# Kernel optimization log

Measured on AMD Instinct MI355X. Metric: run time of the kernel, lower is better.

Reference implementation:

```python
import jax, jax.numpy as jnp
import numpy as np

H = 16      # num_heads = num_channels // head_dim
D = 128     # head_dim
BLK = 64    # NABLA / flex_attention block size
THR = 0.8   # sparse_params['P'] cumulative-density threshold
EPS = 1e-6  # RMSNorm eps


def _rmsnorm(x, w):
    # torch nn.RMSNorm over last dim (computed in fp32 as in norm_qk)
    return x * jax.lax.rsqrt(jnp.mean(x * x, axis=-1, keepdims=True) + EPS) * w


def _rotate_half(x):
    x1, x2 = jnp.split(x, 2, axis=-1)
    return jnp.concatenate([-x2, x1], axis=-1)


def _apply_rotary(x, cos, sin):
    # x: [S, H, D]; cos/sin: [S, 1, D]
    return x * cos + _rotate_half(x) * sin


def _nabla_block_mask(q, k, sta_mask):
    # q, k: [H, S, D] -> block-pooled attention map, cumulative-density threshold
    Hh, S, Dd = q.shape
    nb = S // BLK
    qb = q.reshape(Hh, nb, BLK, Dd).mean(axis=2)           # [H, nQ, D]
    kb = k.reshape(Hh, nb, BLK, Dd).mean(axis=2)           # [H, nK, D]
    p = jax.nn.softmax(jnp.einsum('hqd,hkd->hqk', qb, kb) / np.sqrt(Dd), axis=-1)
    srt = -jnp.sort(-p, axis=-1)                           # descending
    csum = jnp.cumsum(srt, axis=-1)
    keep_sorted = (csum - srt) < THR                       # smallest set covering THR mass
    cutoff = jnp.min(jnp.where(keep_sorted, srt, jnp.inf), axis=-1, keepdims=True)
    return (p >= cutoff) | sta_mask[None]                  # [H, nQ, nK] bool


def reference(x, rope_cos, rope_sin, sta_mask, Wq, bq, Wk, bk, Wv, bv, Wo, bo, qn_w, kn_w):
    S, C = x.shape
    q = (x @ Wq + bq).reshape(S, H, D)
    k = (x @ Wk + bk).reshape(S, H, D)
    v = (x @ Wv + bv).reshape(S, H, D)
    q = _rmsnorm(q, qn_w)
    k = _rmsnorm(k, kn_w)
    q = _apply_rotary(q, rope_cos, rope_sin)
    k = _apply_rotary(k, rope_cos, rope_sin)
    q = q.transpose(1, 0, 2)  # [H, S, D]
    k = k.transpose(1, 0, 2)
    v = v.transpose(1, 0, 2)
    blk_keep = _nabla_block_mask(q, k, sta_mask)                     # [H, nQ, nK]
    mask = jnp.repeat(jnp.repeat(blk_keep, BLK, axis=1), BLK, axis=2)  # [H, S, S]
    scores = jnp.einsum('hqd,hkd->hqk', q, k) / np.sqrt(D)
    scores = jnp.where(mask, scores, -jnp.inf)
    attn = jax.nn.softmax(scores, axis=-1)
    out = jnp.einsum('hqk,hkd->hqd', attn, v)                        # [H, S, D]
    out = out.transpose(1, 0, 2).reshape(S, H * D)
    return out @ Wo + bo


def setup_inputs() -> dict:
    key = jax.random.key(0)
    ks = jax.random.split(key, 12)
    S, C = 2048, 2048
    nb = S // BLK
    sc = 0.02
    return {
        'x': jax.random.normal(ks[0], (S, C), jnp.float32),
        'rope_cos': jax.random.uniform(ks[1], (S, 1, D), jnp.float32),
        'rope_sin': jax.random.uniform(ks[2], (S, 1, D), jnp.float32),
        'sta_mask': jax.random.randint(ks[3], (nb, nb), 0, 2).astype(bool),
        'Wq': jax.random.normal(ks[4], (C, C), jnp.float32) * sc,
        'bq': jnp.zeros((C,), jnp.float32),
        'Wk': jax.random.normal(ks[5], (C, C), jnp.float32) * sc,
        'bk': jnp.zeros((C,), jnp.float32),
        'Wv': jax.random.normal(ks[6], (C, C), jnp.float32) * sc,
        'bv': jnp.zeros((C,), jnp.float32),
        'Wo': jax.random.normal(ks[7], (C, C), jnp.float32) * sc,
        'bo': jnp.zeros((C,), jnp.float32),
        'qn_w': jnp.ones((D,), jnp.float32),
        'kn_w': jnp.ones((D,), jnp.float32),
    }
```

## Files before the change

### kernel.cpp

```cpp
#include <hip/hip_runtime.h>


#define S_LEN 2048
#define CDIM  2048
#define NH    16
#define HD    128
#define NB    32

typedef __attribute__((ext_vector_type(8))) short s8v;
typedef __attribute__((ext_vector_type(4))) short s4v;
typedef __attribute__((ext_vector_type(4))) float f4v;

__device__ __forceinline__ short f2bf(float f){
  unsigned u = __builtin_bit_cast(unsigned, f);
  u += 0x7fffu + ((u>>16)&1u);
  return (short)(u>>16);
}
__device__ __forceinline__ float bf2f(short s){
  unsigned u = ((unsigned)(unsigned short)s)<<16;
  return __builtin_bit_cast(float, u);
}
__device__ __forceinline__ void gload_lds16(const void* g, void* l){
  __builtin_amdgcn_global_load_lds(
      (const __attribute__((address_space(1))) void*)g,
      (__attribute__((address_space(3))) void*)l, 16, 0, 0);
}

__global__ void __launch_bounds__(256) conv_x_kernel(
    const float* __restrict__ x, short* __restrict__ xcat)
{
  int i = blockIdx.x*256 + threadIdx.x;
  f4v v = ((const f4v*)x)[i];
  int s = i >> 9, c4 = (i & 511)*4;
  s4v hi, lo;
#pragma unroll
  for (int e=0;e<4;e++){
    short h = f2bf(v[e]);
    hi[e] = h;
    lo[e] = f2bf(v[e] - bf2f(h));
  }
  short* row = xcat + (size_t)s*6144 + c4;
  *(s4v*)(row)        = hi;
  *(s4v*)(row + 2048) = hi;
  *(s4v*)(row + 4096) = lo;
}

__global__ void __launch_bounds__(256) conv_w3_kernel(
    const float* __restrict__ W, short* __restrict__ wcat)
{
  __shared__ float tile[64][65];
  const int k0 = blockIdx.y*64, n0 = blockIdx.x*64, t = threadIdx.x;
#pragma unroll
  for (int i=0;i<16;i++){
    int idx = i*256 + t, r = idx>>6, c = idx&63;
    tile[r][c] = W[(size_t)(k0+r)*2048 + (n0+c)];
  }
  __syncthreads();
#pragma unroll
  for (int i=0;i<16;i++){
    int idx = i*256 + t, n = idx>>6, k = idx&63;
    float v = tile[k][n];
    short h  = f2bf(v);
    short lo = f2bf(v - bf2f(h));
    short* base = wcat + (size_t)(n0+n)*6144 + (k0+k);
    base[0]    = h;
    base[2048] = lo;
    base[4096] = h;
  }
}

__global__ void __launch_bounds__(256) conv_w1_kernel(
    const float* __restrict__ W, short* __restrict__ wt)
{
  __shared__ float tile[64][65];
  const int k0 = blockIdx.y*64, n0 = blockIdx.x*64, t = threadIdx.x;
#pragma unroll
  for (int i=0;i<16;i++){
    int idx = i*256 + t, r = idx>>6, c = idx&63;
    tile[r][c] = W[(size_t)(k0+r)*2048 + (n0+c)];
  }
  __syncthreads();
#pragma unroll
  for (int i=0;i<16;i++){
    int idx = i*256 + t, n = idx>>6, k = idx&63;
    wt[(size_t)(n0+n)*2048 + (k0+k)] = f2bf(tile[k][n]);
  }
}

template<int OUT>
__global__ void __launch_bounds__(512, 4) gemm8_bt(
    const short* __restrict__ A, int lda,
    const short* __restrict__ Bt, int ldb,
    const float* __restrict__ biasQ, const float* __restrict__ biasK,
    int nsplit,
    void* __restrict__ Cout, int ldc, int K, int ntiles)
{
  __shared__ short Alds[2][128*64];
  __shared__ short Blds[2][128*64];
  const int t = threadIdx.x, w = t>>6, l = t&63;
  const int nwg = gridDim.x;
  const int bid = blockIdx.x;
  const int swz = (bid & 7)*(nwg>>3) + (bid>>3);
  const int mi = swz / ntiles, ni = swz % ntiles;
  const int m0 = mi*128, n0 = ni*128;
  const int wr = w>>2, wc = w&3;
  const int l16 = l&15, lg = l>>4;

  f4v acc[4][2];
  f4v z = {0.f,0.f,0.f,0.f};
#pragma unroll
  for (int a=0;a<4;a++)
#pragma unroll
    for (int b=0;b<2;b++) acc[a][b] = z;

  const int srow = w*16 + (l>>3);
  const int scol = ((l&7) ^ ((l>>3)&7)) * 8;
  const short* Ag = A  + (size_t)(m0 + srow)*lda + scol;
  const short* Bg = Bt + (size_t)(n0 + srow)*ldb + scol;

  auto stageAB = [&](int buf, int kt){
#pragma unroll
    for (int ii=0;ii<2;ii++){
      gload_lds16(Ag + (size_t)ii*8*lda + kt, (char*)Alds[buf] + w*2048 + ii*1024);
      gload_lds16(Bg + (size_t)ii*8*ldb + kt, (char*)Blds[buf] + w*2048 + ii*1024);
    }
  };

  stageAB(0, 0);
  int cur = 0;
  for (int kt = 0; kt < K; kt += 64){
    if (kt + 64 < K){
      stageAB(cur^1, kt+64);
      asm volatile("s_waitcnt vmcnt(4)" ::: "memory");
    } else {
      asm volatile("s_waitcnt vmcnt(0)" ::: "memory");
    }
    __builtin_amdgcn_s_barrier();
    const char* Al = (const char*)Alds[cur];
    const char* Bl = (const char*)Blds[cur];
#pragma unroll
    for (int kk=0;kk<2;kk++){
      const int swx = ((l16&7)<<4);
      s8v af[4], bfv[2];
#pragma unroll
      for (int mt=0;mt<4;mt++)
        af[mt]  = *(const s8v*)(Al + (wr*64+mt*16+l16)*128 + ((kk*64 + lg*16) ^ swx));
#pragma unroll
      for (int jt=0;jt<2;jt++)
        bfv[jt] = *(const s8v*)(Bl + (wc*32+jt*16+l16)*128 + ((kk*64 + lg*16) ^ swx));
      __builtin_amdgcn_s_setprio(1);
#pragma unroll
      for (int mt=0;mt<4;mt++)
#pragma unroll
        for (int jt=0;jt<2;jt++)
          acc[mt][jt] = __builtin_amdgcn_mfma_f32_16x16x32_bf16(
              af[mt], bfv[jt], acc[mt][jt], 0, 0, 0);
      __builtin_amdgcn_s_setprio(0);
    }
    asm volatile("" ::: "memory");
    __builtin_amdgcn_s_barrier();
    cur ^= 1;
  }

  const float* bp = (n0 >= nsplit) ? (biasK + (n0 - nsplit)) : (biasQ + n0);

#pragma unroll
  for (int mt=0;mt<4;mt++)
#pragma unroll
    for (int r=0;r<4;r++){
      int row = m0 + wr*64 + mt*16 + lg*4 + r;
#pragma unroll
      for (int jt=0;jt<2;jt++){
        int cr = wc*32 + jt*16 + l16;
        float v = acc[mt][jt][r] + bp[cr];
        if (OUT == 0) ((float*)Cout)[(size_t)row*ldc + n0 + cr] = v;
        else          ((short*)Cout)[(size_t)row*ldc + n0 + cr] = f2bf(v);
      }
    }
}

__global__ void __launch_bounds__(256) qk_post_kernel(
    const float* __restrict__ QKf,
    const float* __restrict__ qw, const float* __restrict__ kw,
    const float* __restrict__ rc, const float* __restrict__ rs,
    short* __restrict__ Qh, short* __restrict__ Kh,
    float* __restrict__ Qb, float* __restrict__ Kb)
{
  __shared__ float pool[4][128];
  const int sb = blockIdx.x, h = blockIdx.y, which = blockIdx.z;
  const float* in    = QKf + (which ? 2048 : 0);
  const float* wvp   = which ? kw : qw;
  short*       outp  = which ? Kh : Qh;
  float*       poolp = which ? Kb : Qb;
  const int t = threadIdx.x, w = t>>6, l = t&63;
  const int s = sb*64 + w*16 + (l>>2), d0 = (l&3)*32;

  float a[32];
  const f4v* src = (const f4v*)(in + (size_t)s*4096 + h*128 + d0);
#pragma unroll
  for (int i=0;i<8;i++){
    f4v v = src[i];
    a[i*4]=v[0]; a[i*4+1]=v[1]; a[i*4+2]=v[2]; a[i*4+3]=v[3];
  }
  float ss = 0.f;
#pragma unroll
  for (int i=0;i<32;i++) ss += a[i]*a[i];
  ss += __shfl_xor(ss,1); ss += __shfl_xor(ss,2);
  float rstd = 1.0f / sqrtf(ss*(1.0f/128.0f) + 1e-6f);

  const f4v* wv4 = (const f4v*)(wvp + d0);
#pragma unroll
  for (int i=0;i<8;i++){
    f4v wv = wv4[i];
    a[i*4]   *= rstd*wv[0]; a[i*4+1] *= rstd*wv[1];
    a[i*4+2] *= rstd*wv[2]; a[i*4+3] *= rstd*wv[3];
  }
  float cv[32], sv[32];
  const f4v* cs4 = (const f4v*)(rc + (size_t)s*128 + d0);
  const f4v* sn4 = (const f4v*)(rs + (size_t)s*128 + d0);
#pragma unroll
  for (int i=0;i<8;i++){
    f4v c = cs4[i], sn = sn4[i];
    cv[i*4]=c[0]; cv[i*4+1]=c[1]; cv[i*4+2]=c[2]; cv[i*4+3]=c[3];
    sv[i*4]=sn[0]; sv[i*4+1]=sn[1]; sv[i*4+2]=sn[2]; sv[i*4+3]=sn[3];
  }
  const float sgn = (l&2) ? 1.f : -1.f;
#pragma unroll
  for (int i=0;i<32;i++){
    float pv = __shfl_xor(a[i], 2);
    a[i] = a[i]*cv[i] + sgn*pv*sv[i];
  }
  short* op = outp + ((size_t)h*2048 + s)*128 + d0;
#pragma unroll
  for (int c8=0;c8<8;c8++){
    s4v ob;
#pragma unroll
    for (int e=0;e<4;e++) ob[e] = f2bf(a[c8*4+e]);
    ((s4v*)op)[c8] = ob;
  }
#pragma unroll
  for (int i=0;i<32;i++){
    a[i] += __shfl_xor(a[i],4);
    a[i] += __shfl_xor(a[i],8);
    a[i] += __shfl_xor(a[i],16);
    a[i] += __shfl_xor(a[i],32);
  }
  if ((l>>2)==0){
#pragma unroll
    for (int i=0;i<32;i++) pool[w][d0+i] = a[i];
  }
  __syncthreads();
  if (t < 128)
    poolp[((size_t)h*32 + sb)*128 + t] =
        (pool[0][t]+pool[1][t]+pool[2][t]+pool[3][t]) * (1.0f/64.0f);
}

__global__ void __launch_bounds__(64) nabla_mask_kernel(
    const float* __restrict__ Qb, const float* __restrict__ Kb,
    const void* __restrict__ sta, unsigned char* __restrict__ keep)
{
  const int qi = blockIdx.x, h = blockIdx.y, l = threadIdx.x;
  const int j = l & 31;
  const int* si = (const int*)sta;
  int wv0 = si[j];
  int isInt = __all((wv0==0) | (wv0==1));

  const f4v* qr = (const f4v*)(Qb + ((size_t)h*32+qi)*128);
  const f4v* kr = (const f4v*)(Kb + ((size_t)h*32+j)*128);
  float dot = 0.f;
#pragma unroll
  for (int d=0; d<32; d++){
    f4v a = qr[d], b = kr[d];
    dot += a[0]*b[0] + a[1]*b[1] + a[2]*b[2] + a[3]*b[3];
  }
  float logit = dot / sqrtf(128.0f);
  float mx = logit;
  mx = fmaxf(mx, __shfl_xor(mx,1));  mx = fmaxf(mx, __shfl_xor(mx,2));
  mx = fmaxf(mx, __shfl_xor(mx,4));  mx = fmaxf(mx, __shfl_xor(mx,8));
  mx = fmaxf(mx, __shfl_xor(mx,16));
  float e = expf(logit - mx);
  float den = e;
  den += __shfl_xor(den,1);  den += __shfl_xor(den,2);
  den += __shfl_xor(den,4);  den += __shfl_xor(den,8);
  den += __shfl_xor(den,16);
  float p = e / den;
  float Sg = 0.f;
  for (int jj=0;jj<32;jj++){
    float pj = __shfl(p, jj);
    if (pj > p) Sg += pj;
  }
  float cand = (Sg < 0.8f) ? p : 3.0e38f;
  float cut = cand;
  cut = fminf(cut, __shfl_xor(cut,1));  cut = fminf(cut, __shfl_xor(cut,2));
  cut = fminf(cut, __shfl_xor(cut,4));  cut = fminf(cut, __shfl_xor(cut,8));
  cut = fminf(cut, __shfl_xor(cut,16));
  bool stab = isInt ? (si[qi*32+j] != 0)
                    : (((const unsigned char*)sta)[qi*32+j] != 0);
  if (l < 32)
    keep[((size_t)(h*32)+qi)*32 + j] = ((p >= cut) || stab) ? 1 : 0;
}

__global__ void __launch_bounds__(256) v_trans_kernel(
    const short* __restrict__ v_sd, short* __restrict__ vt)
{
  __shared__ short tile[64][65];
  const int sb = blockIdx.x, db = blockIdx.y, h = blockIdx.z, t = threadIdx.x;
#pragma unroll
  for (int i=0;i<16;i++){
    int idx = i*256 + t, r = idx>>6, c = idx&63;
    tile[r][c] = v_sd[(size_t)(sb*64+r)*2048 + h*128 + db*64 + c];
  }
  __syncthreads();
#pragma unroll
  for (int i=0;i<16;i++){
    int idx = i*256 + t, dn = idx>>6, s2 = idx&63;
    vt[((size_t)h*128 + db*64 + dn)*2048 + sb*64 + s2] = tile[s2][dn];
  }
}

__global__ void __launch_bounds__(256) attn_fwd_kernel(
    const short* __restrict__ qh, const short* __restrict__ kh,
    const short* __restrict__ vt, const unsigned char* __restrict__ keep,
    short* __restrict__ attn_out)
{
  __shared__ short Klds[2][64*128];
  __shared__ short Vlds[2][128*64];
  __shared__ short Plds[4][1024];
  const int bid = blockIdx.x;
  const int swz = (bid & 7)*64 + (bid >> 3);
  const int h = swz >> 5, qb = swz & 31;
  const int t = threadIdx.x, w = t>>6, l = t&63;
  const int l16 = l&15, lg = l>>4;

  s8v qf[4];
  const int sq0 = qb*64 + w*16;
  const short* qbase = qh + ((size_t)h*2048 + sq0 + l16)*128 + lg*8;
#pragma unroll
  for (int kf=0;kf<4;kf++) qf[kf] = *(const s8v*)(qbase + kf*32);

  f4v acc[8];
  f4v z = {0.f,0.f,0.f,0.f};
#pragma unroll
  for (int d=0;d<8;d++) acc[d] = z;
  float mrow[4], lsum[4];
#pragma unroll
  for (int r=0;r<4;r++){ mrow[r] = -3.0e38f; lsum[r] = 0.f; }

  const unsigned char* keeprow = keep + ((size_t)(h*32) + qb)*32;
  const short* kg0 = kh + (size_t)h*2048*128;
  const short* vg0 = vt + (size_t)h*128*2048;

  unsigned km = 0;
#pragma unroll
  for (int j=0;j<32;j++) km |= ((unsigned)keeprow[j]) << j;
  if (!km) km = 1;

  auto stageKV = [&](int buf, int j){
    const char* kg = (const char*)(kg0 + (size_t)(j*64)*128);
    const char* vg = (const char*)(vg0 + j*64);
#pragma unroll
    for (int ii=0;ii<4;ii++){
      int kr = (w*4+ii)*4 + (l>>4);
      int ks = ((l&15)*16) ^ ((kr&7)<<4);
      gload_lds16(kg + (size_t)kr*256 + ks, (char*)Klds[buf] + (w*4+ii)*1024);
      int vr = (w*4+ii)*8 + (l>>3);
      int vs = ((l&7)*16) ^ ((vr&7)<<4);
      gload_lds16(vg + (size_t)vr*4096 + vs, (char*)Vlds[buf] + (w*4+ii)*1024);
    }
  };

  asm volatile("s_waitcnt vmcnt(0)" ::: "memory");
  int jcur = (int)__builtin_ctz(km); km &= km-1;
  stageKV(0, jcur);
  int cur = 0;

  while (jcur >= 0){
    int jn = -1;
    if (km){ jn = (int)__builtin_ctz(km); km &= km-1; }
    if (jn >= 0){
      stageKV(cur^1, jn);
      asm volatile("s_waitcnt vmcnt(8)" ::: "memory");
    } else {
      asm volatile("s_waitcnt vmcnt(0)" ::: "memory");
    }
    __builtin_amdgcn_s_barrier();

    const char* Kl = (const char*)Klds[cur];
    const char* Vl = (const char*)Vlds[cur];

    f4v sacc[4];
#pragma unroll
    for (int nt=0;nt<4;nt++) sacc[nt] = z;
    __builtin_amdgcn_s_setprio(1);
#pragma unroll
    for (int kf=0;kf<4;kf++)
#pragma unroll
      for (int nt=0;nt<4;nt++){
        int kr = nt*16 + l16;
        s8v bfr = *(const s8v*)(Kl + ((kr*256 + kf*64 + lg*16) ^ ((kr&7)<<4)));
        sacc[nt] = __builtin_amdgcn_mfma_f32_16x16x32_bf16(qf[kf], bfr, sacc[nt], 0,0,0);
      }
    __builtin_amdgcn_s_setprio(0);
    const float scl = 0.08838834764831845f;
#pragma unroll
    for (int nt=0;nt<4;nt++) sacc[nt] *= scl;

#pragma unroll
    for (int r=0;r<4;r++){
      float mx = fmaxf(fmaxf(sacc[0][r], sacc[1][r]),
                       fmaxf(sacc[2][r], sacc[3][r]));
      mx = fmaxf(mx, __shfl_xor(mx,1));  mx = fmaxf(mx, __shfl_xor(mx,2));
      mx = fmaxf(mx, __shfl_xor(mx,4));  mx = fmaxf(mx, __shfl_xor(mx,8));
      float mnew = fmaxf(mrow[r], mx);
      float resc = __expf(mrow[r] - mnew);
      mrow[r] = mnew;
      float psum = 0.f;
#pragma unroll
      for (int nt=0;nt<4;nt++){
        float p = __expf(sacc[nt][r] - mnew);
        sacc[nt][r] = p;
        psum += p;
      }
      psum += __shfl_xor(psum,1);  psum += __shfl_xor(psum,2);
      psum += __shfl_xor(psum,4);  psum += __shfl_xor(psum,8);
      lsum[r] = lsum[r]*resc + psum;
#pragma unroll
      for (int dt=0;dt<8;dt++) acc[dt][r] *= resc;
    }

    char* Pl = (char*)Plds[w];
#pragma unroll
    for (int nt=0;nt<4;nt++)
#pragma unroll
      for (int r=0;r<4;r++){
        int pr = lg*4 + r;
        *(short*)(Pl + ((pr*128 + nt*32 + l16*2) ^ ((pr&7)<<4))) = f2bf(sacc[nt][r]);
      }
    s8v pa0 = *(const s8v*)(Pl + ((l16*128 +  0 + lg*16) ^ ((l16&7)<<4)));
    s8v pa1 = *(const s8v*)(Pl + ((l16*128 + 64 + lg*16) ^ ((l16&7)<<4)));

    __builtin_amdgcn_s_setprio(1);
#pragma unroll
    for (int kk=0;kk<2;kk++){
      s8v pa = kk ? pa1 : pa0;
#pragma unroll
      for (int dt=0;dt<8;dt++){
        int vr = dt*16 + l16;
        s8v vb = *(const s8v*)(Vl + ((vr*128 + kk*64 + lg*16) ^ ((vr&7)<<4)));
        acc[dt] = __builtin_amdgcn_mfma_f32_16x16x32_bf16(pa, vb, acc[dt], 0,0,0);
      }
    }
    __builtin_amdgcn_s_setprio(0);

    asm volatile("" ::: "memory");
    __builtin_amdgcn_s_barrier();
    cur ^= 1; jcur = jn;
  }

#pragma unroll
  for (int r=0;r<4;r++){
    float inv = 1.0f / lsum[r];
    int s = qb*64 + w*16 + lg*4 + r;
#pragma unroll
    for (int dt=0;dt<8;dt++)
      attn_out[(size_t)s*2048 + h*128 + dt*16 + l16] = f2bf(acc[dt][r]*inv);
  }
}

extern "C" void kernel_launch(void* const* d_in, const int* in_sizes, int n_in,
                              void* d_out, int out_size, void* d_ws, size_t ws_size,
                              hipStream_t stream)
{
  (void)in_sizes; (void)n_in; (void)out_size; (void)ws_size;
  const float* x   = (const float*)d_in[0];
  const float* rc  = (const float*)d_in[1];
  const float* rs  = (const float*)d_in[2];
  const void*  sta = d_in[3];
  const float* Wq  = (const float*)d_in[4];
  const float* bq  = (const float*)d_in[5];
  const float* Wk  = (const float*)d_in[6];
  const float* bk  = (const float*)d_in[7];
  const float* Wv  = (const float*)d_in[8];
  const float* bv  = (const float*)d_in[9];
  const float* Wo  = (const float*)d_in[10];
  const float* bo  = (const float*)d_in[11];
  const float* qnw = (const float*)d_in[12];
  const float* knw = (const float*)d_in[13];

  char* ws = (char*)d_ws;
  size_t off = 0;
  auto take = [&](size_t b){ char* p = ws + off; off = (off + b + 255) & ~(size_t)255; return p; };
  short* Xcat  = (short*)take((size_t)2048*6144*2);
  short* Wcat2 = (short*)take((size_t)4096*6144*2);
  short* Wt1   = (short*)take((size_t)2048*2048*2);
  float* QKf   = (float*)take((size_t)2048*4096*4);
  short* Vsd   = (short*)take((size_t)2048*2048*2);
  short* Qh    = (short*)take((size_t)NH*2048*128*2);
  short* Kh    = (short*)take((size_t)NH*2048*128*2);
  float* Qb    = (float*)take((size_t)NH*32*128*4);
  float* Kb    = (float*)take((size_t)NH*32*128*4);
  unsigned char* Keep = (unsigned char*)take(NH*32*32);
  short* AttnO = (short*)QKf;
  short* Vt    = (short*)((char*)QKf + (size_t)16*1024*1024);

  conv_x_kernel <<<4096, 256, 0, stream>>>(x, Xcat);
  conv_w3_kernel<<<dim3(32,32), 256, 0, stream>>>(Wq, Wcat2);
  conv_w3_kernel<<<dim3(32,32), 256, 0, stream>>>(Wk, Wcat2 + (size_t)2048*6144);
  gemm8_bt<0><<<512, 512, 0, stream>>>(Xcat, 6144, Wcat2, 6144, bq, bk, 2048,
                                       QKf, 4096, 6144, 32);
  conv_w1_kernel<<<dim3(32,32), 256, 0, stream>>>(Wv, Wt1);
  gemm8_bt<1><<<256, 512, 0, stream>>>(Xcat, 6144, Wt1, 2048, bv, bv, 4096,
                                       Vsd, 2048, 2048, 16);
  qk_post_kernel<<<dim3(32,16,2), 256, 0, stream>>>(QKf, qnw, knw, rc, rs, Qh, Kh, Qb, Kb);
  v_trans_kernel<<<dim3(32,2,16), 256, 0, stream>>>(Vsd, Vt);
  nabla_mask_kernel<<<dim3(32,16), 64, 0, stream>>>(Qb, Kb, sta, Keep);
  attn_fwd_kernel<<<512, 256, 0, stream>>>(Qh, Kh, Vt, Keep, AttnO);
  conv_w1_kernel<<<dim3(32,32), 256, 0, stream>>>(Wo, Wt1);
  gemm8_bt<0><<<256, 512, 0, stream>>>((const short*)AttnO, 2048, Wt1, 2048, bo, bo, 4096,
                                       d_out, 2048, 2048, 16);
}
```

Measured before the change: 447.4 us.

## Add dedicated 256x128-tile QK GEMM with deduplicated split-bf16 operand buffers

The split-bf16 (hi/lo) X and W concatenated buffers shrink from three K-segments to two, removing the duplicated hi copy. Segment selection now happens in the load address computation inside a new gemm_qk kernel. That kernel uses a larger 256x128 tile with a 4x4 MFMA accumulator per wave and half the workgroups, to raise data reuse per LDS load and to cut global and LDS traffic for the three-term GEMM. The cost is higher register and LDS pressure, occupancy limited to 2, and fewer workgroups (256) to fill the GPU.

```diff
diff --git a/kernel.cpp b/kernel.cpp
--- a/kernel.cpp
+++ b/kernel.cpp
@@ -39,10 +39,9 @@
     hi[e] = h;
     lo[e] = f2bf(v[e] - bf2f(h));
   }
-  short* row = xcat + (size_t)s*6144 + c4;
+  short* row = xcat + (size_t)s*4096 + c4;
   *(s4v*)(row)        = hi;
-  *(s4v*)(row + 2048) = hi;
-  *(s4v*)(row + 4096) = lo;
+  *(s4v*)(row + 2048) = lo;
 }
 
 __global__ void __launch_bounds__(256) conv_w3_kernel(
@@ -62,10 +61,9 @@
     float v = tile[k][n];
     short h  = f2bf(v);
     short lo = f2bf(v - bf2f(h));
-    short* base = wcat + (size_t)(n0+n)*6144 + (k0+k);
+    short* base = wcat + (size_t)(n0+n)*4096 + (k0+k);
     base[0]    = h;
     base[2048] = lo;
-    base[4096] = h;
   }
 }
 
@@ -85,14 +83,103 @@
     int idx = i*256 + t, n = idx>>6, k = idx&63;
     wt[(size_t)(n0+n)*2048 + (k0+k)] = f2bf(tile[k][n]);
   }
+}
+
+__global__ void __launch_bounds__(512, 2) gemm_qk(
+    const short* __restrict__ A,
+    const short* __restrict__ Bt,
+    const float* __restrict__ bq, const float* __restrict__ bk,
+    float* __restrict__ Cout)
+{
+  __shared__ short Alds[2][256*64];
+  __shared__ short Blds[2][128*64];
+  const int t = threadIdx.x, w = t>>6, l = t&63;
+  const int bid = blockIdx.x;
+  const int swz = (bid & 7)*32 + (bid >> 3);
+  const int m0 = (swz >> 5)*256, n0 = (swz & 31)*128;
+  const int wr = w>>1, wc = w&1;
+  const int l16 = l&15, lg = l>>4;
+
+  f4v acc[4][4];
+  f4v z = {0.f,0.f,0.f,0.f};
+#pragma unroll
+  for (int a=0;a<4;a++)
+#pragma unroll
+    for (int b=0;b<4;b++) acc[a][b] = z;
+
+  const int srA = w*32 + (l>>3);
+  const int srB = w*16 + (l>>3);
+  const int scol = ((l&7) ^ ((l>>3)&7)) * 8;
+  const short* Ag = A  + (size_t)(m0 + srA)*4096 + scol;
+  const short* Bg = Bt + (size_t)(n0 + srB)*4096 + scol;
+
+  auto stage = [&](int buf, int kt){
+    const int ak = (kt < 2048) ? kt : kt - 2048;
+    const int bk2 = (kt < 4096) ? kt : kt - 4096;
+#pragma unroll
+    for (int ii=0;ii<4;ii++)
+      gload_lds16(Ag + (size_t)ii*8*4096 + ak, (char*)Alds[buf] + w*4096 + ii*1024);
+#pragma unroll
+    for (int ii=0;ii<2;ii++)
+      gload_lds16(Bg + (size_t)ii*8*4096 + bk2, (char*)Blds[buf] + w*2048 + ii*1024);
+  };
+
+  stage(0, 0);
+  int cur = 0;
+  for (int kt = 0; kt < 6144; kt += 64){
+    if (kt + 64 < 6144){
+      stage(cur^1, kt+64);
+      asm volatile("s_waitcnt vmcnt(6)" ::: "memory");
+    } else {
+      asm volatile("s_waitcnt vmcnt(0)" ::: "memory");
+    }
+    __builtin_amdgcn_s_barrier();
+    const char* Al = (const char*)Alds[cur];
+    const char* Bl = (const char*)Blds[cur];
+#pragma unroll
+    for (int kk=0;kk<2;kk++){
+      const int swx = ((l16&7)<<4);
+      const int koff = (kk*64 + lg*16);
+      s8v af[4], bfv[4];
+#pragma unroll
+      for (int mt=0;mt<4;mt++)
+        af[mt]  = *(const s8v*)(Al + (wr*64+mt*16+l16)*128 + (koff ^ swx));
+#pragma unroll
+      for (int nt=0;nt<4;nt++)
+        bfv[nt] = *(const s8v*)(Bl + (wc*64+nt*16+l16)*128 + (koff ^ swx));
+      __builtin_amdgcn_s_setprio(1);
+#pragma unroll
+      for (int mt=0;mt<4;mt++)
+#pragma unroll
+        for (int nt=0;nt<4;nt++)
+          acc[mt][nt] = __builtin_amdgcn_mfma_f32_16x16x32_bf16(
+              af[mt], bfv[nt], acc[mt][nt], 0, 0, 0);
+      __builtin_amdgcn_s_setprio(0);
+    }
+    asm volatile("" ::: "memory");
+    __builtin_amdgcn_s_barrier();
+    cur ^= 1;
+  }
+
+  const float* bp = (n0 >= 2048) ? (bk + (n0 - 2048)) : (bq + n0);
+#pragma unroll
+  for (int mt=0;mt<4;mt++)
+#pragma unroll
+    for (int r=0;r<4;r++){
+      int row = m0 + wr*64 + mt*16 + lg*4 + r;
+#pragma unroll
+      for (int nt=0;nt<4;nt++){
+        int cr = wc*64 + nt*16 + l16;
+        Cout[(size_t)row*4096 + n0 + cr] = acc[mt][nt][r] + bp[cr];
+      }
+    }
 }
 
 template<int OUT>
 __global__ void __launch_bounds__(512, 4) gemm8_bt(
     const short* __restrict__ A, int lda,
     const short* __restrict__ Bt, int ldb,
-    const float* __restrict__ biasQ, const float* __restrict__ biasK,
-    int nsplit,
+    const float* __restrict__ bias,
     void* __restrict__ Cout, int ldc, int K, int ntiles)
 {
   __shared__ short Alds[2][128*64];
@@ -162,8 +249,6 @@
     cur ^= 1;
   }
 
-  const float* bp = (n0 >= nsplit) ? (biasK + (n0 - nsplit)) : (biasQ + n0);
-
 #pragma unroll
   for (int mt=0;mt<4;mt++)
 #pragma unroll
@@ -172,7 +257,7 @@
 #pragma unroll
       for (int jt=0;jt<2;jt++){
         int cr = wc*32 + jt*16 + l16;
-        float v = acc[mt][jt][r] + bp[cr];
+        float v = acc[mt][jt][r] + bias[n0 + cr];
         if (OUT == 0) ((float*)Cout)[(size_t)row*ldc + n0 + cr] = v;
         else          ((short*)Cout)[(size_t)row*ldc + n0 + cr] = f2bf(v);
       }
@@ -490,8 +575,8 @@
   char* ws = (char*)d_ws;
   size_t off = 0;
   auto take = [&](size_t b){ char* p = ws + off; off = (off + b + 255) & ~(size_t)255; return p; };
-  short* Xcat  = (short*)take((size_t)2048*6144*2);
-  short* Wcat2 = (short*)take((size_t)4096*6144*2);
+  short* Xcat  = (short*)take((size_t)2048*4096*2);
+  short* Wcat2 = (short*)take((size_t)4096*4096*2);
   short* Wt1   = (short*)take((size_t)2048*2048*2);
   float* QKf   = (float*)take((size_t)2048*4096*4);
   short* Vsd   = (short*)take((size_t)2048*2048*2);
@@ -505,17 +590,14 @@
 
   conv_x_kernel <<<4096, 256, 0, stream>>>(x, Xcat);
   conv_w3_kernel<<<dim3(32,32), 256, 0, stream>>>(Wq, Wcat2);
-  conv_w3_kernel<<<dim3(32,32), 256, 0, stream>>>(Wk, Wcat2 + (size_t)2048*6144);
-  gemm8_bt<0><<<512, 512, 0, stream>>>(Xcat, 6144, Wcat2, 6144, bq, bk, 2048,
-                                       QKf, 4096, 6144, 32);
+  conv_w3_kernel<<<dim3(32,32), 256, 0, stream>>>(Wk, Wcat2 + (size_t)2048*4096);
+  gemm_qk<<<256, 512, 0, stream>>>(Xcat, Wcat2, bq, bk, QKf);
   conv_w1_kernel<<<dim3(32,32), 256, 0, stream>>>(Wv, Wt1);
-  gemm8_bt<1><<<256, 512, 0, stream>>>(Xcat, 6144, Wt1, 2048, bv, bv, 4096,
-                                       Vsd, 2048, 2048, 16);
+  gemm8_bt<1><<<256, 512, 0, stream>>>(Xcat, 4096, Wt1, 2048, bv, Vsd, 2048, 2048, 16);
   qk_post_kernel<<<dim3(32,16,2), 256, 0, stream>>>(QKf, qnw, knw, rc, rs, Qh, Kh, Qb, Kb);
   v_trans_kernel<<<dim3(32,2,16), 256, 0, stream>>>(Vsd, Vt);
   nabla_mask_kernel<<<dim3(32,16), 64, 0, stream>>>(Qb, Kb, sta, Keep);
   attn_fwd_kernel<<<512, 256, 0, stream>>>(Qh, Kh, Vt, Keep, AttnO);
   conv_w1_kernel<<<dim3(32,32), 256, 0, stream>>>(Wo, Wt1);
-  gemm8_bt<0><<<256, 512, 0, stream>>>((const short*)AttnO, 2048, Wt1, 2048, bo, bo, 4096,
-                                       d_out, 2048, 2048, 16);
-}
+  gemm8_bt<0><<<256, 512, 0, stream>>>((const short*)AttnO, 2048, Wt1, 2048, bo, d_out, 2048, 2048, 16);
+}
```

New measurement: 476.6 us. 1.07x slower.
